# Kernel optimization log

Measured on AMD Instinct MI355X. Metric: run time of the kernel, lower is better.

Reference implementation:

```python
import jax, jax.numpy as jnp
import numpy as np

NT, NH, NW = 16, 16, 16
HEADS, DIM_HEAD = 8, 64
DIM = 512
DEPTH = 4
EPS = 1e-5


def _layernorm(x, g, b):
    mu = jnp.mean(x, axis=-1, keepdims=True)
    var = jnp.mean(jnp.square(x - mu), axis=-1, keepdims=True)
    return (x - mu) * jax.lax.rsqrt(var + EPS) * g + b


def setup_inputs() -> dict:
    key = jax.random.key(0)
    ks = jax.random.split(key, 4)
    n = NT * NH * NW
    inner = HEADS * DIM_HEAD
    x = jax.random.normal(ks[0], (8, n, DIM), dtype=jnp.float32)
    Wqkv = jax.random.normal(ks[1], (DEPTH, DIM, 3 * inner), dtype=jnp.float32) * (DIM ** -0.5)
    Wout = jax.random.normal(ks[2], (DEPTH, inner, DIM), dtype=jnp.float32) * (inner ** -0.5)
    bout = jnp.zeros((DEPTH, DIM), dtype=jnp.float32)
    gamma = jnp.ones((DEPTH, DIM), dtype=jnp.float32)
    beta = jnp.zeros((DEPTH, DIM), dtype=jnp.float32)
    return {"x": x, "Wqkv": Wqkv, "Wout": Wout, "bout": bout, "gamma": gamma, "beta": beta}


def _fda_layer(x, Wqkv, Wout, bout, g, bb):
    b, n, d = x.shape
    hs = HEADS // 2
    s = NH * NW
    scale = DIM_HEAD ** -0.5
    y = _layernorm(x, g, bb)
    qkv = y @ Wqkv  # (b, n, 3*inner)
    q, k, v = jnp.split(qkv, 3, axis=-1)
    # b n (h d) -> b h n d
    def to_heads(t):
        return t.reshape(b, n, HEADS, DIM_HEAD).transpose(0, 2, 1, 3)
    q, k, v = to_heads(q), to_heads(k), to_heads(v)
    # spatial branch: first half of heads, view n as (t, s)
    qs = q[:, :hs].reshape(b, hs, NT, s, DIM_HEAD)
    ks = k[:, :hs].reshape(b, hs, NT, s, DIM_HEAD)
    vs = v[:, :hs].reshape(b, hs, NT, s, DIM_HEAD)
    sp_dots = jnp.einsum('bhtid,bhtjd->bhtij', qs, ks) * scale
    sp_attn = jax.nn.softmax(sp_dots, axis=-1)
    sp_out = jnp.einsum('bhtij,bhtjd->bhtid', sp_attn, vs)  # (b,hs,nt,s,dh)
    # temporal branch: second half of heads, view n as (s, t)
    qt = q[:, hs:].reshape(b, hs, s, NT, DIM_HEAD)
    kt = k[:, hs:].reshape(b, hs, s, NT, DIM_HEAD)
    vt = v[:, hs:].reshape(b, hs, s, NT, DIM_HEAD)
    tp_dots = jnp.einsum('bhsid,bhsjd->bhsij', qt, kt) * scale
    tp_attn = jax.nn.softmax(tp_dots, axis=-1)
    tp_out = jnp.einsum('bhsij,bhsjd->bhsid', tp_attn, vt)  # (b,hs,s,nt,dh)
    out = jnp.concatenate([sp_out.reshape(b, hs, n, DIM_HEAD),
                           tp_out.reshape(b, hs, n, DIM_HEAD)], axis=1)  # (b,h,n,dh)
    out = out.transpose(0, 2, 1, 3).reshape(b, n, HEADS * DIM_HEAD)
    return out @ Wout + bout


def reference(x, Wqkv, Wout, bout, gamma, beta):
    for l in range(DEPTH):
        x = _fda_layer(x, Wqkv[l], Wout[l], bout[l], gamma[l], beta[l]) + x
    return x
```

## Files before the change

### kernel.cpp

```cpp
#include <hip/hip_runtime.h>
#include <hip/hip_bf16.h>

typedef __bf16 bf16x8 __attribute__((ext_vector_type(8)));
typedef float f32x4 __attribute__((ext_vector_type(4)));

#define AS1(p) ((const __attribute__((address_space(1))) void*)(p))
#define AS3(p) ((__attribute__((address_space(3))) void*)(p))

__global__ __launch_bounds__(256) void transpose32(const float* __restrict__ W,
                                                   __bf16* __restrict__ WT,
                                                   int K, int N) {
  __shared__ float t[32][33];
  int l = blockIdx.z;
  int k0 = blockIdx.y * 32, n0 = blockIdx.x * 32;
  int tx = threadIdx.x & 31, ty = threadIdx.x >> 5;
  const float* src = W + ((size_t)l * K + k0) * N + n0;
#pragma unroll
  for (int i = 0; i < 32; i += 8) t[ty + i][tx] = src[(size_t)(ty + i) * N + tx];
  __syncthreads();
  __bf16* dst = WT + ((size_t)l * N + n0) * K + k0;
#pragma unroll
  for (int i = 0; i < 32; i += 8) dst[(size_t)(ty + i) * K + tx] = (__bf16)t[tx][ty + i];
}

__global__ __launch_bounds__(256) void ln_kernel(const float* __restrict__ x,
                                                 const float* __restrict__ gamma,
                                                 const float* __restrict__ beta,
                                                 __bf16* __restrict__ y) {
  int wave = threadIdx.x >> 6, lane = threadIdx.x & 63;
  size_t row = (size_t)blockIdx.x * 4 + wave;
  const float* xr = x + row * 512 + lane * 8;
  float4 v0 = *(const float4*)xr;
  float4 v1 = *(const float4*)(xr + 4);
  float s = v0.x + v0.y + v0.z + v0.w + v1.x + v1.y + v1.z + v1.w;
  float ss = v0.x * v0.x + v0.y * v0.y + v0.z * v0.z + v0.w * v0.w +
             v1.x * v1.x + v1.y * v1.y + v1.z * v1.z + v1.w * v1.w;
#pragma unroll
  for (int m = 1; m < 64; m <<= 1) {
    s += __shfl_xor(s, m);
    ss += __shfl_xor(ss, m);
  }
  float mean = s * (1.f / 512.f);
  float var = ss * (1.f / 512.f) - mean * mean;
  float rstd = rsqrtf(var + 1e-5f);
  const float* gp = gamma + lane * 8;
  const float* bp = beta + lane * 8;
  float4 g0 = *(const float4*)gp, g1 = *(const float4*)(gp + 4);
  float4 b0 = *(const float4*)bp, b1 = *(const float4*)(bp + 4);
  bf16x8 o;
  o[0] = (__bf16)((v0.x - mean) * rstd * g0.x + b0.x);
  o[1] = (__bf16)((v0.y - mean) * rstd * g0.y + b0.y);
  o[2] = (__bf16)((v0.z - mean) * rstd * g0.z + b0.z);
  o[3] = (__bf16)((v0.w - mean) * rstd * g0.w + b0.w);
  o[4] = (__bf16)((v1.x - mean) * rstd * g1.x + b1.x);
  o[5] = (__bf16)((v1.y - mean) * rstd * g1.y + b1.y);
  o[6] = (__bf16)((v1.z - mean) * rstd * g1.z + b1.z);
  o[7] = (__bf16)((v1.w - mean) * rstd * g1.w + b1.w);
  *(bf16x8*)(y + row * 512 + lane * 8) = o;
}

#define STAGE_PART(kt_, part_)                                                   \
  {                                                                              \
    const __bf16* gb_ = ((part_) < 2) ? Abase : Bbase;                           \
    int rowoff_ = ((part_)&1) * 128;                                             \
    const __bf16* g0_ = gb_ + (size_t)(rowoff_ + r0s) * 512 + (kt_)*64 + s0 * 8; \
    const __bf16* g1_ = gb_ + (size_t)(rowoff_ + r1s) * 512 + (kt_)*64 + s1 * 8; \
    char* lb_ = lds + (((kt_)&1) * 65536) + ((part_)*16384);                     \
    __builtin_amdgcn_global_load_lds(AS1(g0_), AS3(lb_ + ldsw0), 16, 0, 0);      \
    __builtin_amdgcn_global_load_lds(AS1(g1_), AS3(lb_ + ldsw1), 16, 0, 0);      \
  }

template <int NCOLS>
__global__ __launch_bounds__(512, 2) void gemm256(const __bf16* __restrict__ A,
                                                  const __bf16* __restrict__ BT,
                                                  __bf16* __restrict__ Cb) {
  extern __shared__ __attribute__((aligned(128))) char lds[];
  constexpr int NT = NCOLS / 256;
  int bid = blockIdx.x;
  int cpx = gridDim.x >> 3;
  int L = (bid & 7) * cpx + (bid >> 3);
  int tileM = L / NT, tileN = L - tileM * NT;
  int tid = threadIdx.x;
  int l = tid & 63, w = tid >> 6;
  int lm = l & 15, lh = l >> 4;
  int wave_m = w >> 2, wave_n = w & 3;
  const __bf16* Abase = A + (size_t)tileM * 256 * 512;
  const __bf16* Bbase = BT + (size_t)tileN * 256 * 512;
  int r0s = tid >> 3, s0 = (tid & 7) ^ (r0s & 7);
  int p1 = tid + 512;
  int r1s = p1 >> 3, s1 = (p1 & 7) ^ (r1s & 7);
  int ldsw0 = (w * 64) * 16, ldsw1 = (512 + w * 64) * 16;

  f32x4 acc[8][4];
#pragma unroll
  for (int m = 0; m < 8; ++m)
#pragma unroll
    for (int n = 0; n < 4; ++n) acc[m][n] = (f32x4){0.f, 0.f, 0.f, 0.f};

  int xorv = (lm & 7) << 4;
  int kb0 = (lh * 16) ^ xorv;
  int kb1 = (64 + lh * 16) ^ xorv;
  int arow = wave_m * 128 + lm;
  int brow = wave_n * 64 + lm;

  STAGE_PART(0, 0); STAGE_PART(0, 1); STAGE_PART(0, 2); STAGE_PART(0, 3);

  for (int kt = 0; kt < 8; ++kt) {
    char* sb = lds + (kt & 1) * 65536;
    if (kt < 7) {
      STAGE_PART(kt + 1, 0);
      asm volatile("s_waitcnt vmcnt(2)" ::: "memory");
    } else {
      asm volatile("s_waitcnt vmcnt(0)" ::: "memory");
    }
    __builtin_amdgcn_sched_barrier(0);
    __builtin_amdgcn_s_barrier();
    bf16x8 bfrag[4][2];
#pragma unroll
    for (int nf = 0; nf < 4; ++nf) {
      const char* bp = sb + 32768 + (brow + nf * 16) * 128;
      bfrag[nf][0] = *(const bf16x8*)(bp + kb0);
      bfrag[nf][1] = *(const bf16x8*)(bp + kb1);
    }
#pragma unroll
    for (int ph = 0; ph < 4; ++ph) {
      bf16x8 af[2][2];
#pragma unroll
      for (int m = 0; m < 2; ++m) {
        const char* ap = sb + (arow + (ph * 2 + m) * 16) * 128;
        af[m][0] = *(const bf16x8*)(ap + kb0);
        af[m][1] = *(const bf16x8*)(ap + kb1);
      }
      if (ph == 0 && kt < 7) STAGE_PART(kt + 1, 1);
      if (ph == 1 && kt < 7) STAGE_PART(kt + 1, 2);
      if (ph == 2 && kt < 7) STAGE_PART(kt + 1, 3);
      __builtin_amdgcn_s_setprio(1);
#pragma unroll
      for (int m = 0; m < 2; ++m)
#pragma unroll
        for (int nf = 0; nf < 4; ++nf) {
          acc[ph * 2 + m][nf] = __builtin_amdgcn_mfma_f32_16x16x32_bf16(
              af[m][0], bfrag[nf][0], acc[ph * 2 + m][nf], 0, 0, 0);
          acc[ph * 2 + m][nf] = __builtin_amdgcn_mfma_f32_16x16x32_bf16(
              af[m][1], bfrag[nf][1], acc[ph * 2 + m][nf], 0, 0, 0);
        }
      __builtin_amdgcn_s_setprio(0);
    }
    __builtin_amdgcn_s_barrier();
  }

  __syncthreads();
  __bf16* lw = (__bf16*)(lds + w * 16384);
#pragma unroll
  for (int mf = 0; mf < 8; ++mf)
#pragma unroll
    for (int nf = 0; nf < 4; ++nf)
#pragma unroll
      for (int r = 0; r < 4; ++r)
        lw[(mf * 16 + lh * 4 + r) * 64 + nf * 16 + lm] = (__bf16)acc[mf][nf][r];
  asm volatile("s_waitcnt lgkmcnt(0)" ::: "memory");
  __builtin_amdgcn_sched_barrier(0);
  int crow0 = tileM * 256 + wave_m * 128;
  int ccol = tileN * 256 + wave_n * 64 + (l & 7) * 8;
#pragma unroll
  for (int p = 0; p < 16; ++p) {
    int lrow = p * 8 + (l >> 3);
    bf16x8 v = *(const bf16x8*)&lw[lrow * 64 + (l & 7) * 8];
    *(bf16x8*)&Cb[(size_t)(crow0 + lrow) * NCOLS + ccol] = v;
  }
}

#define STAGE128(kt_, part_)                                                    \
  {                                                                             \
    const __bf16* gb_ = ((part_) == 0) ? Abase : Bbase;                         \
    const __bf16* g0_ = gb_ + (size_t)r0s * 512 + (kt_)*64 + s0 * 8;            \
    const __bf16* g1_ = gb_ + (size_t)r1s * 512 + (kt_)*64 + s1 * 8;            \
    char* lb_ = lds + (((kt_)&1) * 32768) + ((part_)*16384);                    \
    __builtin_amdgcn_global_load_lds(AS1(g0_), AS3(lb_ + ldsw0), 16, 0, 0);     \
    __builtin_amdgcn_global_load_lds(AS1(g1_), AS3(lb_ + ldsw1), 16, 0, 0);     \
  }

__global__ __launch_bounds__(512, 4) void gemm128res(const __bf16* __restrict__ A,
                                                     const __bf16* __restrict__ BT,
                                                     float* Cf,
                                                     const float* __restrict__ bias,
                                                     const float* Resid) {
  extern __shared__ __attribute__((aligned(128))) char lds[];
  constexpr int NCOLS = 512;
  constexpr int NT = 4;
  int bid = blockIdx.x;
  int cpx = gridDim.x >> 3;
  int L = (bid & 7) * cpx + (bid >> 3);
  int tileM = L / NT, tileN = L - tileM * NT;
  int tid = threadIdx.x;
  int l = tid & 63, w = tid >> 6;
  int lm = l & 15, lh = l >> 4;
  int wave_m = w >> 2, wave_n = w & 3;
  const __bf16* Abase = A + (size_t)tileM * 128 * 512;
  const __bf16* Bbase = BT + (size_t)tileN * 128 * 512;
  int r0s = tid >> 3, s0 = (tid & 7) ^ (r0s & 7);
  int p1 = tid + 512;
  int r1s = p1 >> 3, s1 = (p1 & 7) ^ (r1s & 7);
  int ldsw0 = (w * 64) * 16, ldsw1 = 8192 + (w * 64) * 16;

  f32x4 acc[4][2];
#pragma unroll
  for (int m = 0; m < 4; ++m)
#pragma unroll
    for (int n = 0; n < 2; ++n) acc[m][n] = (f32x4){0.f, 0.f, 0.f, 0.f};

  int xorv = (lm & 7) << 4;
  int kb0 = (lh * 16) ^ xorv;
  int kb1 = (64 + lh * 16) ^ xorv;
  int arow = wave_m * 64 + lm;
  int brow = wave_n * 32 + lm;

  STAGE128(0, 0); STAGE128(0, 1);

  for (int kt = 0; kt < 8; ++kt) {
    char* sb = lds + (kt & 1) * 32768;
    if (kt < 7) {
      STAGE128(kt + 1, 0);
      asm volatile("s_waitcnt vmcnt(2)" ::: "memory");
    } else {
      asm volatile("s_waitcnt vmcnt(0)" ::: "memory");
    }
    __builtin_amdgcn_sched_barrier(0);
    __builtin_amdgcn_s_barrier();
    bf16x8 bfrag[2][2];
#pragma unroll
    for (int nf = 0; nf < 2; ++nf) {
      const char* bp = sb + 16384 + (brow + nf * 16) * 128;
      bfrag[nf][0] = *(const bf16x8*)(bp + kb0);
      bfrag[nf][1] = *(const bf16x8*)(bp + kb1);
    }
    bf16x8 af[4][2];
#pragma unroll
    for (int mf = 0; mf < 4; ++mf) {
      const char* ap = sb + (arow + mf * 16) * 128;
      af[mf][0] = *(const bf16x8*)(ap + kb0);
      af[mf][1] = *(const bf16x8*)(ap + kb1);
    }
    if (kt < 7) STAGE128(kt + 1, 1);
    __builtin_amdgcn_s_setprio(1);
#pragma unroll
    for (int mf = 0; mf < 4; ++mf)
#pragma unroll
      for (int nf = 0; nf < 2; ++nf) {
        acc[mf][nf] = __builtin_amdgcn_mfma_f32_16x16x32_bf16(af[mf][0], bfrag[nf][0],
                                                              acc[mf][nf], 0, 0, 0);
        acc[mf][nf] = __builtin_amdgcn_mfma_f32_16x16x32_bf16(af[mf][1], bfrag[nf][1],
                                                              acc[mf][nf], 0, 0, 0);
      }
    __builtin_amdgcn_s_setprio(0);
    __builtin_amdgcn_s_barrier();
  }

  float* lf = (float*)(lds + w * 2560);
  int crow0 = tileM * 128 + wave_m * 64;
  int ccol0 = tileN * 128 + wave_n * 32;
  int erow = l >> 2;
  int ecl = (l & 3) * 8;
  float4 ba = *(const float4*)(bias + ccol0 + ecl);
  float4 bb = *(const float4*)(bias + ccol0 + ecl + 4);
#pragma unroll
  for (int mf = 0; mf < 4; ++mf) {
#pragma unroll
    for (int nf = 0; nf < 2; ++nf)
#pragma unroll
      for (int r = 0; r < 4; ++r)
        lf[(lh * 4 + r) * 40 + nf * 16 + lm] = acc[mf][nf][r];
    size_t rowg = (size_t)(crow0 + mf * 16 + erow);
    const float* rp = Resid + rowg * NCOLS + ccol0 + ecl;
    float* cp = Cf + rowg * NCOLS + ccol0 + ecl;
    float4 a0 = *(float4*)&lf[erow * 40 + ecl];
    float4 a1 = *(float4*)&lf[erow * 40 + ecl + 4];
    float4 r0 = *(const float4*)rp;
    float4 r1 = *(const float4*)(rp + 4);
    float4 o0, o1;
    o0.x = a0.x + ba.x + r0.x; o0.y = a0.y + ba.y + r0.y;
    o0.z = a0.z + ba.z + r0.z; o0.w = a0.w + ba.w + r0.w;
    o1.x = a1.x + bb.x + r1.x; o1.y = a1.y + bb.y + r1.y;
    o1.z = a1.z + bb.z + r1.z; o1.w = a1.w + bb.w + r1.w;
    *(float4*)cp = o0;
    *(float4*)(cp + 4) = o1;
  }
}

__global__ __launch_bounds__(256) void attn_spatial(const __bf16* __restrict__ qkv,
                                                    __bf16* __restrict__ attn_out) {
  __shared__ __attribute__((aligned(16))) __bf16 VT[64 * 256];
  __shared__ __attribute__((aligned(16))) __bf16 P[4][4096];
  int bid = blockIdx.x;
  int b = bid >> 6;
  int rem = bid & 63;
  int h = rem >> 4;
  int t = rem & 15;
  int tid = threadIdx.x;
  int w = tid >> 6, l = tid & 63;
  size_t nbase = (size_t)b * 4096 + t * 256;
#pragma unroll
  for (int i = 0; i < 8; i++) {
    int idx = tid + i * 256;
    int key = idx >> 3, dseg = idx & 7;
    bf16x8 v = *(const bf16x8*)(qkv + (nbase + key) * 1536 + 1024 + h * 64 + dseg * 8);
#pragma unroll
    for (int d2 = 0; d2 < 8; d2++) {
      int dh = dseg * 8 + d2;
      VT[dh * 256 + (((key >> 3) ^ (dh & 7)) << 3) + (key & 7)] = v[d2];
    }
  }
  __syncthreads();
  int lm = l & 15, lh = l >> 4;
  for (int it = 0; it < 4; ++it) {
    int qbase = it * 64 + w * 16;
    const __bf16* qp = qkv + (nbase + qbase + lm) * 1536 + h * 64 + lh * 8;
    bf16x8 aq0 = *(const bf16x8*)qp;
    bf16x8 aq1 = *(const bf16x8*)(qp + 32);
    f32x4 sa[16];
#pragma unroll
    for (int tn = 0; tn < 16; ++tn) {
      const __bf16* kp = qkv + (nbase + tn * 16 + lm) * 1536 + 512 + h * 64 + lh * 8;
      bf16x8 bk0 = *(const bf16x8*)kp;
      bf16x8 bk1 = *(const bf16x8*)(kp + 32);
      f32x4 z = {0.f, 0.f, 0.f, 0.f};
      z = __builtin_amdgcn_mfma_f32_16x16x32_bf16(aq0, bk0, z, 0, 0, 0);
      sa[tn] = __builtin_amdgcn_mfma_f32_16x16x32_bf16(aq1, bk1, z, 0, 0, 0);
    }
    float rmax[4] = {-1e30f, -1e30f, -1e30f, -1e30f};
#pragma unroll
    for (int tn = 0; tn < 16; ++tn)
#pragma unroll
      for (int r = 0; r < 4; ++r) {
        sa[tn][r] *= 0.125f;
        rmax[r] = fmaxf(rmax[r], sa[tn][r]);
      }
#pragma unroll
    for (int m = 1; m < 16; m <<= 1)
#pragma unroll
      for (int r = 0; r < 4; ++r) rmax[r] = fmaxf(rmax[r], __shfl_xor(rmax[r], m));
    float rsum[4] = {0.f, 0.f, 0.f, 0.f};
#pragma unroll
    for (int tn = 0; tn < 16; ++tn)
#pragma unroll
      for (int r = 0; r < 4; ++r) {
        float e = __expf(sa[tn][r] - rmax[r]);
        sa[tn][r] = e;
        rsum[r] += e;
      }
#pragma unroll
    for (int m = 1; m < 16; m <<= 1)
#pragma unroll
      for (int r = 0; r < 4; ++r) rsum[r] += __shfl_xor(rsum[r], m);
    float rinv[4];
#pragma unroll
    for (int r = 0; r < 4; ++r) rinv[r] = 1.f / rsum[r];
#pragma unroll
    for (int tn = 0; tn < 16; ++tn)
#pragma unroll
      for (int r = 0; r < 4; ++r) {
        int row = lh * 4 + r;
        int col = tn * 16 + lm;
        P[w][row * 256 + ((((col >> 3)) ^ (row & 7)) << 3) + (col & 7)] =
            (__bf16)(sa[tn][r] * rinv[r]);
      }
    f32x4 oa[4];
#pragma unroll
    for (int nt = 0; nt < 4; ++nt) oa[nt] = (f32x4){0.f, 0.f, 0.f, 0.f};
#pragma unroll
    for (int kc = 0; kc < 8; ++kc) {
      bf16x8 pa = *(const bf16x8*)&P[w][lm * 256 + (((kc * 4 + lh) ^ (lm & 7)) << 3)];
#pragma unroll
      for (int nt = 0; nt < 4; ++nt) {
        int dh = nt * 16 + lm;
        bf16x8 bv = *(const bf16x8*)&VT[dh * 256 + (((kc * 4 + lh) ^ (dh & 7)) << 3)];
        oa[nt] = __builtin_amdgcn_mfma_f32_16x16x32_bf16(pa, bv, oa[nt], 0, 0, 0);
      }
    }
#pragma unroll
    for (int nt = 0; nt < 4; ++nt)
#pragma unroll
      for (int r = 0; r < 4; ++r) {
        size_t row = nbase + qbase + lh * 4 + r;
        attn_out[row * 512 + h * 64 + nt * 16 + lm] = (__bf16)oa[nt][r];
      }
  }
}

__global__ __launch_bounds__(256) void attn_temporal(const __bf16* __restrict__ qkv,
                                                     __bf16* __restrict__ attn_out) {
  __shared__ __attribute__((aligned(16))) __bf16 VT[4][64 * 40];
  __shared__ __attribute__((aligned(16))) __bf16 P[4][16 * 40];
  int tid = threadIdx.x;
  {
    float4 z4 = {0.f, 0.f, 0.f, 0.f};
#pragma unroll
    for (int i = 0; i < 5; ++i) ((float4*)&VT[0][0])[tid + i * 256] = z4;
    if (tid < 64) ((float4*)&P[0][0])[tid + 256] = z4;
    ((float4*)&P[0][0])[tid] = z4;
  }
  __syncthreads();
  int bid = blockIdx.x;
  int b = bid >> 8;
  int rem = bid & 255;
  int h = 4 + (rem >> 6);
  int g = rem & 63;
  int w = tid >> 6, l = tid & 63;
  int lm = l & 15, lh = l >> 4;
  int sid = g * 4 + w;
  size_t n0 = (size_t)b * 4096 + sid * 16;

  const __bf16* qp = qkv + (n0 + lm) * 1536 + h * 64 + lh * 8;
  bf16x8 aq0 = *(const bf16x8*)qp;
  bf16x8 aq1 = *(const bf16x8*)(qp + 32);
  const __bf16* kp = qp + 512;
  bf16x8 bk0 = *(const bf16x8*)kp;
  bf16x8 bk1 = *(const bf16x8*)(kp + 32);
  int kk = l >> 2;
  int dh0 = (l & 3) * 8;
  const __bf16* vp = qkv + (n0 + kk) * 1536 + 1024 + h * 64 + dh0;
  bf16x8 vr0 = *(const bf16x8*)vp;
  bf16x8 vr1 = *(const bf16x8*)(vp + 32);

  f32x4 s4 = {0.f, 0.f, 0.f, 0.f};
  s4 = __builtin_amdgcn_mfma_f32_16x16x32_bf16(aq0, bk0, s4, 0, 0, 0);
  s4 = __builtin_amdgcn_mfma_f32_16x16x32_bf16(aq1, bk1, s4, 0, 0, 0);

#pragma unroll
  for (int d2 = 0; d2 < 8; ++d2) VT[w][(dh0 + d2) * 40 + kk] = vr0[d2];
#pragma unroll
  for (int d2 = 0; d2 < 8; ++d2) VT[w][(dh0 + 32 + d2) * 40 + kk] = vr1[d2];

  float e[4];
  float rmax[4];
#pragma unroll
  for (int r = 0; r < 4; ++r) {
    e[r] = s4[r] * 0.125f;
    rmax[r] = e[r];
  }
#pragma unroll
  for (int m = 1; m < 16; m <<= 1)
#pragma unroll
    for (int r = 0; r < 4; ++r) rmax[r] = fmaxf(rmax[r], __shfl_xor(rmax[r], m));
  float rsum[4];
#pragma unroll
  for (int r = 0; r < 4; ++r) {
    e[r] = __expf(e[r] - rmax[r]);
    rsum[r] = e[r];
  }
#pragma unroll
  for (int m = 1; m < 16; m <<= 1)
#pragma unroll
    for (int r = 0; r < 4; ++r) rsum[r] += __shfl_xor(rsum[r], m);
#pragma unroll
  for (int r = 0; r < 4; ++r)
    P[w][(lh * 4 + r) * 40 + lm] = (__bf16)(e[r] / rsum[r]);

  asm volatile("s_waitcnt lgkmcnt(0)" ::: "memory");
  __builtin_amdgcn_sched_barrier(0);

  bf16x8 pa = *(const bf16x8*)&P[w][lm * 40 + lh * 8];
#pragma unroll
  for (int nt = 0; nt < 4; ++nt) {
    bf16x8 bv = *(const bf16x8*)&VT[w][(nt * 16 + lm) * 40 + lh * 8];
    f32x4 oa = {0.f, 0.f, 0.f, 0.f};
    oa = __builtin_amdgcn_mfma_f32_16x16x32_bf16(pa, bv, oa, 0, 0, 0);
#pragma unroll
    for (int r = 0; r < 4; ++r)
      attn_out[(n0 + lh * 4 + r) * 512 + h * 64 + nt * 16 + lm] = (__bf16)oa[r];
  }
}

extern "C" void kernel_launch(void* const* d_in, const int* in_sizes, int n_in,
                              void* d_out, int out_size, void* d_ws, size_t ws_size,
                              hipStream_t stream) {
  const float* x = (const float*)d_in[0];
  const float* Wqkv = (const float*)d_in[1];
  const float* Wout = (const float*)d_in[2];
  const float* bout = (const float*)d_in[3];
  const float* gamma = (const float*)d_in[4];
  const float* beta = (const float*)d_in[5];
  float* out = (float*)d_out;

  const size_t OFF_WOUT = 6291456;
  const size_t OFF_Y = OFF_WOUT + 2097152;
  const size_t OFF_QKV = OFF_Y + 33554432;
  const size_t NEEDED = OFF_QKV + 100663296;
  if (ws_size < NEEDED) return;
  char* ws = (char*)d_ws;
  __bf16* WqkvT = (__bf16*)ws;
  __bf16* WoutT = (__bf16*)(ws + OFF_WOUT);
  __bf16* ybuf = (__bf16*)(ws + OFF_Y);
  __bf16* qkv = (__bf16*)(ws + OFF_QKV);

  hipFuncSetAttribute((const void*)gemm256<1536>,
                      hipFuncAttributeMaxDynamicSharedMemorySize, 131072);
  hipFuncSetAttribute((const void*)gemm128res,
                      hipFuncAttributeMaxDynamicSharedMemorySize, 65536);

  transpose32<<<dim3(48, 16, 4), 256, 0, stream>>>(Wqkv, WqkvT, 512, 1536);
  transpose32<<<dim3(16, 16, 4), 256, 0, stream>>>(Wout, WoutT, 512, 512);

  for (int layer = 0; layer < 4; ++layer) {
    const float* src = (layer == 0) ? x : out;
    ln_kernel<<<8192, 256, 0, stream>>>(src, gamma + layer * 512, beta + layer * 512, ybuf);
    gemm256<1536><<<768, 512, 131072, stream>>>(
        ybuf, WqkvT + (size_t)layer * 1536 * 512, qkv);
    attn_spatial<<<512, 256, 0, stream>>>(qkv, ybuf);
    attn_temporal<<<2048, 256, 0, stream>>>(qkv, ybuf);
    gemm128res<<<1024, 512, 65536, stream>>>(
        ybuf, WoutT + (size_t)layer * 512 * 512, out, bout + layer * 512, src);
  }
}
```

Baseline: 654.6 us.

## Restructure QKV GEMM to four-stage K=32 pipeline with padded epilogue

```diff
diff --git a/kernel.cpp b/kernel.cpp
--- a/kernel.cpp
+++ b/kernel.cpp
@@ -59,15 +59,15 @@
   *(bf16x8*)(y + row * 512 + lane * 8) = o;
 }
 
-#define STAGE_PART(kt_, part_)                                                   \
-  {                                                                              \
-    const __bf16* gb_ = ((part_) < 2) ? Abase : Bbase;                           \
-    int rowoff_ = ((part_)&1) * 128;                                             \
-    const __bf16* g0_ = gb_ + (size_t)(rowoff_ + r0s) * 512 + (kt_)*64 + s0 * 8; \
-    const __bf16* g1_ = gb_ + (size_t)(rowoff_ + r1s) * 512 + (kt_)*64 + s1 * 8; \
-    char* lb_ = lds + (((kt_)&1) * 65536) + ((part_)*16384);                     \
-    __builtin_amdgcn_global_load_lds(AS1(g0_), AS3(lb_ + ldsw0), 16, 0, 0);      \
-    __builtin_amdgcn_global_load_lds(AS1(g1_), AS3(lb_ + ldsw1), 16, 0, 0);      \
+#define STAGE32(kt_)                                                            \
+  {                                                                             \
+    char* lb_ = lds + (((kt_)&3) * 32768);                                      \
+    const __bf16* ga0_ = Abase + (size_t)rA * 512 + (kt_)*32 + sw8;             \
+    const __bf16* gb0_ = Bbase + (size_t)rA * 512 + (kt_)*32 + sw8;             \
+    __builtin_amdgcn_global_load_lds(AS1(ga0_), AS3(lb_ + dA0), 16, 0, 0);      \
+    __builtin_amdgcn_global_load_lds(AS1(ga0_ + 65536), AS3(lb_ + dA1), 16, 0, 0); \
+    __builtin_amdgcn_global_load_lds(AS1(gb0_), AS3(lb_ + dB0), 16, 0, 0);      \
+    __builtin_amdgcn_global_load_lds(AS1(gb0_ + 65536), AS3(lb_ + dB1), 16, 0, 0); \
   }
 
 template <int NCOLS>
@@ -86,10 +86,10 @@
   int wave_m = w >> 2, wave_n = w & 3;
   const __bf16* Abase = A + (size_t)tileM * 256 * 512;
   const __bf16* Bbase = BT + (size_t)tileN * 256 * 512;
-  int r0s = tid >> 3, s0 = (tid & 7) ^ (r0s & 7);
-  int p1 = tid + 512;
-  int r1s = p1 >> 3, s1 = (p1 & 7) ^ (r1s & 7);
-  int ldsw0 = (w * 64) * 16, ldsw1 = (512 + w * 64) * 16;
+  int rA = tid >> 2;
+  int sw8 = (((tid & 3) ^ ((tid >> 3) & 3)) << 3);
+  int dA0 = w * 1024, dA1 = 8192 + w * 1024;
+  int dB0 = 16384 + w * 1024, dB1 = 24576 + w * 1024;
 
   f32x4 acc[8][4];
 #pragma unroll
@@ -97,76 +97,68 @@
 #pragma unroll
     for (int n = 0; n < 4; ++n) acc[m][n] = (f32x4){0.f, 0.f, 0.f, 0.f};
 
-  int xorv = (lm & 7) << 4;
-  int kb0 = (lh * 16) ^ xorv;
-  int kb1 = (64 + lh * 16) ^ xorv;
+  int kb = ((lh ^ ((lm >> 1) & 3)) << 4);
   int arow = wave_m * 128 + lm;
   int brow = wave_n * 64 + lm;
 
-  STAGE_PART(0, 0); STAGE_PART(0, 1); STAGE_PART(0, 2); STAGE_PART(0, 3);
-
-  for (int kt = 0; kt < 8; ++kt) {
-    char* sb = lds + (kt & 1) * 65536;
-    if (kt < 7) {
-      STAGE_PART(kt + 1, 0);
-      asm volatile("s_waitcnt vmcnt(2)" ::: "memory");
+  STAGE32(0); STAGE32(1); STAGE32(2);
+
+  for (int kt = 0; kt < 16; ++kt) {
+    char* sb = lds + ((kt & 3) * 32768);
+    if (kt < 13) {
+      STAGE32(kt + 3);
+      asm volatile("s_waitcnt vmcnt(12)" ::: "memory");
+    } else if (kt == 13) {
+      asm volatile("s_waitcnt vmcnt(8)" ::: "memory");
+    } else if (kt == 14) {
+      asm volatile("s_waitcnt vmcnt(4)" ::: "memory");
     } else {
       asm volatile("s_waitcnt vmcnt(0)" ::: "memory");
     }
     __builtin_amdgcn_sched_barrier(0);
     __builtin_amdgcn_s_barrier();
-    bf16x8 bfrag[4][2];
-#pragma unroll
-    for (int nf = 0; nf < 4; ++nf) {
-      const char* bp = sb + 32768 + (brow + nf * 16) * 128;
-      bfrag[nf][0] = *(const bf16x8*)(bp + kb0);
-      bfrag[nf][1] = *(const bf16x8*)(bp + kb1);
-    }
-#pragma unroll
-    for (int ph = 0; ph < 4; ++ph) {
-      bf16x8 af[2][2];
-#pragma unroll
-      for (int m = 0; m < 2; ++m) {
-        const char* ap = sb + (arow + (ph * 2 + m) * 16) * 128;
-        af[m][0] = *(const bf16x8*)(ap + kb0);
-        af[m][1] = *(const bf16x8*)(ap + kb1);
-      }
-      if (ph == 0 && kt < 7) STAGE_PART(kt + 1, 1);
-      if (ph == 1 && kt < 7) STAGE_PART(kt + 1, 2);
-      if (ph == 2 && kt < 7) STAGE_PART(kt + 1, 3);
-      __builtin_amdgcn_s_setprio(1);
-#pragma unroll
-      for (int m = 0; m < 2; ++m)
-#pragma unroll
-        for (int nf = 0; nf < 4; ++nf) {
-          acc[ph * 2 + m][nf] = __builtin_amdgcn_mfma_f32_16x16x32_bf16(
-              af[m][0], bfrag[nf][0], acc[ph * 2 + m][nf], 0, 0, 0);
-          acc[ph * 2 + m][nf] = __builtin_amdgcn_mfma_f32_16x16x32_bf16(
-              af[m][1], bfrag[nf][1], acc[ph * 2 + m][nf], 0, 0, 0);
-        }
-      __builtin_amdgcn_s_setprio(0);
-    }
+    bf16x8 bfrag[4];
+#pragma unroll
+    for (int nf = 0; nf < 4; ++nf)
+      bfrag[nf] = *(const bf16x8*)(sb + 16384 + (brow + nf * 16) * 64 + kb);
+    __builtin_amdgcn_s_setprio(1);
+#pragma unroll
+    for (int mf = 0; mf < 8; ++mf) {
+      bf16x8 af = *(const bf16x8*)(sb + (arow + mf * 16) * 64 + kb);
+#pragma unroll
+      for (int nf = 0; nf < 4; ++nf)
+        acc[mf][nf] = __builtin_amdgcn_mfma_f32_16x16x32_bf16(af, bfrag[nf],
+                                                              acc[mf][nf], 0, 0, 0);
+    }
+    __builtin_amdgcn_s_setprio(0);
     __builtin_amdgcn_s_barrier();
   }
 
   __syncthreads();
-  __bf16* lw = (__bf16*)(lds + w * 16384);
-#pragma unroll
-  for (int mf = 0; mf < 8; ++mf)
-#pragma unroll
-    for (int nf = 0; nf < 4; ++nf)
-#pragma unroll
-      for (int r = 0; r < 4; ++r)
-        lw[(mf * 16 + lh * 4 + r) * 64 + nf * 16 + lm] = (__bf16)acc[mf][nf][r];
-  asm volatile("s_waitcnt lgkmcnt(0)" ::: "memory");
-  __builtin_amdgcn_sched_barrier(0);
+  __bf16* lw = (__bf16*)(lds + w * 9216);
   int crow0 = tileM * 256 + wave_m * 128;
   int ccol = tileN * 256 + wave_n * 64 + (l & 7) * 8;
 #pragma unroll
-  for (int p = 0; p < 16; ++p) {
-    int lrow = p * 8 + (l >> 3);
-    bf16x8 v = *(const bf16x8*)&lw[lrow * 64 + (l & 7) * 8];
-    *(bf16x8*)&Cb[(size_t)(crow0 + lrow) * NCOLS + ccol] = v;
+  for (int half = 0; half < 2; ++half) {
+#pragma unroll
+    for (int m2 = 0; m2 < 4; ++m2) {
+      int mf = half * 4 + m2;
+#pragma unroll
+      for (int nf = 0; nf < 4; ++nf)
+#pragma unroll
+        for (int r = 0; r < 4; ++r)
+          lw[(m2 * 16 + lh * 4 + r) * 72 + nf * 16 + lm] = (__bf16)acc[mf][nf][r];
+    }
+    asm volatile("s_waitcnt lgkmcnt(0)" ::: "memory");
+    __builtin_amdgcn_sched_barrier(0);
+#pragma unroll
+    for (int p = 0; p < 8; ++p) {
+      int lrow = p * 8 + (l >> 3);
+      bf16x8 v = *(const bf16x8*)&lw[lrow * 72 + (l & 7) * 8];
+      *(bf16x8*)&Cb[(size_t)(crow0 + half * 64 + lrow) * NCOLS + ccol] = v;
+    }
+    asm volatile("s_waitcnt lgkmcnt(0)" ::: "memory");
+    __builtin_amdgcn_sched_barrier(0);
   }
 }
 
```

Measured after the change: 687.0 us. +4.9%, slower.
